# Kernel optimization log

Hardware: AMD Instinct MI355X
Metric: run time of the kernel (lower is better)

The kernel has to match this reference:

```python
import jax, jax.numpy as jnp
import numpy as np

B, LT, LI, D, H, K = 32, 512, 576, 768, 8, 512


def setup_inputs() -> dict:
    key = jax.random.key(0)
    ks = jax.random.split(key, 10)
    s = 0.02
    return {
        "text_hidden_states": jax.random.normal(ks[0], (B, LT, D), jnp.float32),
        "image_hidden_states": jax.random.normal(ks[1], (B, LI, D), jnp.float32),
        "text_mask": jnp.ones((B, LT), jnp.int32),
        "Wb": jax.random.normal(ks[2], (H, D, D), jnp.float32) * s,   # per-head Linear weights [out,in]
        "Wv": jax.random.normal(ks[3], (K, D), jnp.float32) * s,
        "Wq": jax.random.normal(ks[4], (K, D), jnp.float32) * s,
        "Whv": jax.random.normal(ks[5], (K,), jnp.float32) * s,
        "Whq": jax.random.normal(ks[6], (K,), jnp.float32) * s,
        "Wo": jax.random.normal(ks[7], (D, D * H), jnp.float32) * s,  # output_proj weight [out,in]
        "bo": jnp.zeros((D,), jnp.float32),
    }


def reference(text_hidden_states, image_hidden_states, text_mask, Wb, Wv, Wq, Whv, Whq, Wo, bo):
    text, image = text_hidden_states, image_hidden_states
    # per-head text projection (torch Linear: x @ W.T), batched over heads
    pt = jnp.einsum('bxe,hfe->hbxf', text, Wb)                 # [H,B,LT,D]
    aff = jnp.einsum('hbxe,bye->hbxy', pt, image)              # [H,B,LT,LI]
    wv_v = jnp.einsum('bye,ke->byk', image, Wv)                # [B,LI,K] (head-shared)
    wq_q = jnp.einsum('bxe,ke->bxk', text, Wq)                 # [B,LT,K]
    wqqc = jnp.einsum('bxk,hbxy->hbyk', wq_q, aff)             # [H,B,LI,K]
    wvvc = jnp.einsum('byk,hbxy->hbxk', wv_v, aff)             # [H,B,LT,K]
    h_v = jnp.tanh(wv_v[None] + wqqc)
    h_q = jnp.tanh(wq_q[None] + wvvc)
    att_v = jax.nn.softmax(jnp.einsum('hbyk,k->hby', h_v, Whv), axis=-1)  # over image tokens
    att_q = jax.nn.softmax(jnp.einsum('hbxk,k->hbx', h_q, Whq), axis=-1)  # over text tokens
    ctx_v = jnp.einsum('hby,byd->hbd', att_v, image)
    ctx_q = jnp.einsum('hbx,bxd->hbd', att_q, text)
    head_out = ctx_v + ctx_q                                   # [H,B,D]
    combined = jnp.transpose(head_out, (1, 0, 2)).reshape(text.shape[0], -1)  # [B,H*D]
    return combined @ Wo.T + bo
```

## Files before the change

kernel.cpp:

```cpp
#include <hip/hip_runtime.h>
#include <math.h>

#define B_  32
#define LT_ 512
#define LI_ 576
#define LIP 640
#define D_  768
#define H_  8
#define K_  512
#define NTOK  (LI_ + LT_)
#define CSPLIT 8
#define TPB   (NTOK / CSPLIT)
#define NHEAD ((long)H_ * B_ * D_)

typedef __attribute__((ext_vector_type(4))) short short4v;
typedef __attribute__((ext_vector_type(8))) unsigned short ushort8;
typedef __attribute__((ext_vector_type(8))) _Float16 f16x8;
typedef __attribute__((ext_vector_type(4))) float f32x4;

__device__ __forceinline__ unsigned short f2h(float x) {
  _Float16 h = (_Float16)x;
  return __builtin_bit_cast(unsigned short, h);
}
__device__ __forceinline__ float h2f(unsigned short u) {
  return (float)__builtin_bit_cast(_Float16, u);
}
__device__ __forceinline__ float ftanh(float x) {
  float e = __expf(2.f * x);
  return 1.f - 2.f * __builtin_amdgcn_rcpf(e + 1.f);
}

__device__ __forceinline__ void gl_lds16(const void* g, void* l) {
  __builtin_amdgcn_global_load_lds(
      (const __attribute__((address_space(1))) void*)g,
      (__attribute__((address_space(3))) void*)l, 16, 0, 0);
}

#define EPI_PLAIN 0
#define EPI_T     1
#define EPI_TANH  2
#define EPI_OUT   3

struct Seg {
  const unsigned short *A, *B;
  unsigned short *C, *CT;
  const unsigned short* base;
  const float* wvec;
  float* outv;
  long sA, sB, sC, sCT, sBase;
  int Kd, lda, ldb;
  int gx, gy, nblk, epi, Mlim, valid, ldc, ldt;
};
struct Params { Seg s0, s1, s2; };

__global__ __launch_bounds__(256, 2) void mfma_seg(Params p)
{
  const int orig = blockIdx.x, nwg = gridDim.x;
  const int q8 = nwg >> 3, r8 = nwg & 7;
  const int xcd = orig & 7, idx = orig >> 3;
  const int wg = (xcd < r8 ? xcd * (q8 + 1) : r8 * (q8 + 1) + (xcd - r8) * q8) + idx;

  Seg sg; int local;
  if (wg < p.s0.nblk)                      { sg = p.s0; local = wg; }
  else if (wg < p.s0.nblk + p.s1.nblk)     { sg = p.s1; local = wg - p.s0.nblk; }
  else                                     { sg = p.s2; local = wg - p.s0.nblk - p.s1.nblk; }

  const int bx = local % sg.gx;
  const int tmp2 = local / sg.gx;
  const int by = tmp2 % sg.gy, bz = tmp2 / sg.gy;

  __shared__ unsigned short LDSU[24576];

  const int t = threadIdx.x, lane = t & 63, w = t >> 6;
  const int wr = w >> 1, wc = w & 1;
  const int m0 = bx * 256, n0 = by * 128;
  const int Kd = sg.Kd, lda = sg.lda, ldb = sg.ldb, ldc = sg.ldc;
  const unsigned short* A  = sg.A + (long)bz * sg.sA;
  const unsigned short* Bm = sg.B + (long)bz * sg.sB;

  const int rowb = w * 16 + (lane >> 2);
  const int cswz = ((lane & 3) ^ ((rowb >> 1) & 3)) * 8;
  const bool clampA = (m0 + 256 > sg.Mlim);
  const unsigned short* aSrc = A  + (long)(m0 + rowb) * lda + cswz;
  const unsigned short* bSrc = Bm + (long)(n0 + rowb) * ldb + cswz;
  const int ldsLane = rowb * 32;

  f32x4 acc[8][4];
  #pragma unroll
  for (int i = 0; i < 8; ++i)
    #pragma unroll
    for (int j = 0; j < 4; ++j)
      acc[i][j] = (f32x4){0.f, 0.f, 0.f, 0.f};

  const int rl = lane & 15, g = lane >> 4;
  const int aslot = (g ^ ((rl >> 1) & 3)) << 3;

  auto stage = [&](int bufi, int k0) {
    unsigned short* Ab = LDSU + bufi * 12288;
    unsigned short* Bb = Ab + 8192;
    if (!clampA) {
      #pragma unroll
      for (int q = 0; q < 4; ++q)
        gl_lds16(aSrc + (long)q * 64 * lda + k0, Ab + ldsLane + q * 2048);
    } else {
      #pragma unroll
      for (int q = 0; q < 4; ++q) {
        int rgl = m0 + q * 64 + rowb;
        if (rgl >= sg.Mlim) rgl = sg.Mlim - 1;
        gl_lds16(A + (long)rgl * lda + cswz + k0, Ab + ldsLane + q * 2048);
      }
    }
    #pragma unroll
    for (int q = 0; q < 2; ++q)
      gl_lds16(bSrc + (long)q * 64 * ldb + k0, Bb + ldsLane + q * 2048);
  };

  const int nt = Kd >> 5;
  stage(0, 0);
  __syncthreads();
  int cur = 0;
  for (int tt = 0; tt < nt; ++tt) {
    if (tt + 1 < nt) stage(cur ^ 1, (tt + 1) << 5);
    const unsigned short* Ab = LDSU + cur * 12288;
    const unsigned short* Bb = Ab + 8192;
    f16x8 af[8], bf[4];
    #pragma unroll
    for (int i = 0; i < 8; ++i)
      af[i] = *(const f16x8*)&Ab[(wr * 128 + i * 16 + rl) * 32 + aslot];
    #pragma unroll
    for (int j = 0; j < 4; ++j)
      bf[j] = *(const f16x8*)&Bb[(wc * 64 + j * 16 + rl) * 32 + aslot];
    __builtin_amdgcn_s_setprio(1);
    #pragma unroll
    for (int i = 0; i < 8; ++i)
      #pragma unroll
      for (int j = 0; j < 4; ++j)
        acc[i][j] = __builtin_amdgcn_mfma_f32_16x16x32_f16(af[i], bf[j], acc[i][j], 0, 0, 0);
    __builtin_amdgcn_s_setprio(0);
    __syncthreads();
    cur ^= 1;
  }

  const int rg = lane >> 4;
  if (sg.epi <= EPI_T) {
    unsigned short* C = sg.C + (long)bz * sg.sC;
    #pragma unroll
    for (int i = 0; i < 8; ++i)
      #pragma unroll
      for (int j = 0; j < 4; ++j)
        #pragma unroll
        for (int rr = 0; rr < 4; ++rr) {
          int ml = wr * 128 + i * 16 + rg * 4 + rr;
          int nl = wc * 64 + j * 16 + rl;
          if (m0 + ml < sg.Mlim)
            C[(long)(m0 + ml) * ldc + n0 + nl] = f2h(acc[i][j][rr]);
        }
    if (sg.epi == EPI_T) {
      unsigned short* CT = sg.CT + (long)bz * sg.sCT;
      __syncthreads();
      #pragma unroll
      for (int pp = 0; pp < 2; ++pp) {
        if (wr == pp) {
          #pragma unroll
          for (int i = 0; i < 8; ++i)
            #pragma unroll
            for (int j = 0; j < 4; ++j) {
              int nl = wc * 64 + j * 16 + rl;
              int mh = i * 16 + rg * 4;
              *(short4v*)&LDSU[nl * 136 + mh] = (short4v){
                  (short)f2h(acc[i][j][0]), (short)f2h(acc[i][j][1]),
                  (short)f2h(acc[i][j][2]), (short)f2h(acc[i][j][3])};
            }
        }
        __syncthreads();
        #pragma unroll
        for (int rr = 0; rr < 8; ++rr) {
          int rn = rr * 16 + (t >> 4);
          int m8 = (t & 15) * 8;
          int mg = m0 + pp * 128 + m8;
          if (mg < sg.Mlim)
            *(ushort8*)(CT + (long)(n0 + rn) * sg.ldt + mg) =
                *(const ushort8*)&LDSU[rn * 136 + m8];
        }
        __syncthreads();
      }
    }
  } else if (sg.epi == EPI_TANH) {
    const unsigned short* base = sg.base + (long)bz * sg.sBase;
    float* outp = sg.outv + (long)bz * sg.valid;
    #pragma unroll
    for (int i = 0; i < 8; ++i)
      #pragma unroll
      for (int rr = 0; rr < 4; ++rr) {
        int row = m0 + wr * 128 + i * 16 + rg * 4 + rr;
        if (row < sg.Mlim) {
          float s = 0.f;
          #pragma unroll
          for (int j = 0; j < 4; ++j) {
            int col = n0 + wc * 64 + j * 16 + rl;
            float v = acc[i][j][rr] + h2f(base[(long)row * ldc + col]);
            s += ftanh(v) * sg.wvec[col];
          }
          s += __shfl_xor(s, 1, 64);
          s += __shfl_xor(s, 2, 64);
          s += __shfl_xor(s, 4, 64);
          s += __shfl_xor(s, 8, 64);
          if (rl == 0 && row < sg.valid)
            atomicAdd(&outp[row], s);
        }
      }
  } else {
    float* outp = sg.outv;
    if (wr == 0) {
      #pragma unroll
      for (int i = 0; i < 2; ++i)
        #pragma unroll
        for (int rr = 0; rr < 4; ++rr) {
          int row = i * 16 + rg * 4 + rr;
          #pragma unroll
          for (int j = 0; j < 4; ++j) {
            int col = n0 + wc * 64 + j * 16 + rl;
            atomicAdd(&outp[(long)row * ldc + col], acc[i][j][rr]);
          }
        }
    }
  }
}

struct CSeg { const float* src; unsigned short* dst; long n8; };

__global__ __launch_bounds__(256) void cast_multi(
    CSeg c0, CSeg c1, CSeg c2, CSeg c3, CSeg c4)
{
  long i = (long)blockIdx.x * 256 + threadIdx.x;
  const float* src; unsigned short* dst;
  if      (i < c0.n8)                 { src = c0.src; dst = c0.dst; }
  else if ((i -= c0.n8) < c1.n8)      { src = c1.src; dst = c1.dst; }
  else if ((i -= c1.n8) < c2.n8)      { src = c2.src; dst = c2.dst; }
  else if ((i -= c2.n8) < c3.n8)      { src = c3.src; dst = c3.dst; }
  else if ((i -= c3.n8) < c4.n8)      { src = c4.src; dst = c4.dst; }
  else return;
  float4 v0 = ((const float4*)src)[i * 2];
  float4 v1 = ((const float4*)src)[i * 2 + 1];
  ushort8 o;
  o[0] = f2h(v0.x); o[1] = f2h(v0.y); o[2] = f2h(v0.z); o[3] = f2h(v0.w);
  o[4] = f2h(v1.x); o[5] = f2h(v1.y); o[6] = f2h(v1.z); o[7] = f2h(v1.w);
  *(ushort8*)(dst + i * 8) = o;
}

__global__ __launch_bounds__(256) void cast_pad_image(
    const float* __restrict__ in, unsigned short* __restrict__ out)
{
  long tid = (long)blockIdx.x * 256 + threadIdx.x;
  const long tot = (long)B_ * LIP * (D_ / 8);
  if (tid >= tot) return;
  int e8 = (int)(tid % (D_ / 8));
  long rw = tid / (D_ / 8);
  int y  = (int)(rw % LIP);
  long b = rw / LIP;
  ushort8 o;
  if (y < LI_) {
    const float* p = in + ((b * LI_ + y) * D_ + e8 * 8);
    float4 v0 = *(const float4*)p, v1 = *(const float4*)(p + 4);
    o[0] = f2h(v0.x); o[1] = f2h(v0.y); o[2] = f2h(v0.z); o[3] = f2h(v0.w);
    o[4] = f2h(v1.x); o[5] = f2h(v1.y); o[6] = f2h(v1.z); o[7] = f2h(v1.w);
  } else {
    #pragma unroll
    for (int j = 0; j < 8; ++j) o[j] = 0;
  }
  *(ushort8*)(out + rw * D_ + e8 * 8) = o;
}

__global__ __launch_bounds__(256) void zero_f32(float* __restrict__ p, long n) {
  long i = (long)blockIdx.x * 256 + threadIdx.x;
  if (i < n) p[i] = 0.f;
}

__global__ __launch_bounds__(256) void init_out(
    const float* __restrict__ bo, float* __restrict__ out)
{
  int i = blockIdx.x * 256 + threadIdx.x;
  out[i] = bo[i % D_];
}

__global__ __launch_bounds__(256) void softmax_att(
    const float* __restrict__ lv, const float* __restrict__ lq,
    float* __restrict__ attvG, float* __restrict__ attqG)
{
  const int b = blockIdx.x, h = blockIdx.y;
  const int t = threadIdx.x;
  __shared__ float buf[LI_];
  __shared__ float red[4];

  const float* lvp = lv + ((long)h * B_ + b) * LI_;
  float m = -1e30f;
  for (int i = t; i < LI_; i += 256) m = fmaxf(m, lvp[i]);
  #pragma unroll
  for (int o = 32; o > 0; o >>= 1) m = fmaxf(m, __shfl_down(m, o, 64));
  if ((t & 63) == 0) red[t >> 6] = m;
  __syncthreads();
  m = fmaxf(fmaxf(red[0], red[1]), fmaxf(red[2], red[3]));
  __syncthreads();
  float s = 0.f;
  for (int i = t; i < LI_; i += 256) { float e = __expf(lvp[i] - m); buf[i] = e; s += e; }
  #pragma unroll
  for (int o = 32; o > 0; o >>= 1) s += __shfl_down(s, o, 64);
  if ((t & 63) == 0) red[t >> 6] = s;
  __syncthreads();
  s = red[0] + red[1] + red[2] + red[3];
  {
    float inv = 1.f / s;
    float* op = attvG + ((long)h * B_ + b) * LI_;
    for (int i = t; i < LI_; i += 256) op[i] = buf[i] * inv;
  }
  __syncthreads();

  const float* lqp = lq + ((long)h * B_ + b) * LT_;
  m = -1e30f;
  for (int i = t; i < LT_; i += 256) m = fmaxf(m, lqp[i]);
  #pragma unroll
  for (int o = 32; o > 0; o >>= 1) m = fmaxf(m, __shfl_down(m, o, 64));
  if ((t & 63) == 0) red[t >> 6] = m;
  __syncthreads();
  m = fmaxf(fmaxf(red[0], red[1]), fmaxf(red[2], red[3]));
  __syncthreads();
  s = 0.f;
  for (int i = t; i < LT_; i += 256) { float e = __expf(lqp[i] - m); buf[i] = e; s += e; }
  #pragma unroll
  for (int o = 32; o > 0; o >>= 1) s += __shfl_down(s, o, 64);
  if ((t & 63) == 0) red[t >> 6] = s;
  __syncthreads();
  s = red[0] + red[1] + red[2] + red[3];
  {
    float inv = 1.f / s;
    float* op = attqG + ((long)h * B_ + b) * LT_;
    for (int i = t; i < LT_; i += 256) op[i] = buf[i] * inv;
  }
}

__global__ __launch_bounds__(256) void ctx_part(
    const float* __restrict__ attvG, const float* __restrict__ attqG,
    const unsigned short* __restrict__ text_h,
    float* __restrict__ head_part)
{
  const int b = blockIdx.x, d0 = blockIdx.y * 128, s = blockIdx.z;
  const int t = threadIdx.x, dl = t & 127, g = t >> 7;
  const long IMG_OFF = (long)B_ * LT_ * D_;
  __shared__ float wts[H_][TPB];
  __shared__ long  roff[TPB];
  __shared__ float red[H_][128];
  const int tok0 = s * TPB;
  for (int i = t; i < H_ * TPB; i += 256) {
    int h = i / TPB, j = i % TPB, tok = tok0 + j;
    wts[h][j] = tok < LI_ ? attvG[((long)h * B_ + b) * LI_ + tok]
                          : attqG[((long)h * B_ + b) * LT_ + (tok - LI_)];
  }
  if (t < TPB) {
    int tok = tok0 + t;
    roff[t] = tok < LI_ ? IMG_OFF + ((long)b * LIP + tok) * D_
                        : ((long)b * LT_ + (tok - LI_)) * D_;
  }
  __syncthreads();
  float acc[H_];
  #pragma unroll
  for (int h = 0; h < H_; ++h) acc[h] = 0.f;
  #pragma unroll 4
  for (int j = g; j < TPB; j += 2) {
    float val = h2f(text_h[roff[j] + d0 + dl]);
    #pragma unroll
    for (int h = 0; h < H_; ++h) acc[h] = fmaf(wts[h][j], val, acc[h]);
  }
  if (g == 1) {
    #pragma unroll
    for (int h = 0; h < H_; ++h) red[h][dl] = acc[h];
  }
  __syncthreads();
  if (g == 0) {
    float* hp = head_part + (long)s * NHEAD;
    #pragma unroll
    for (int h = 0; h < H_; ++h)
      hp[((long)h * B_ + b) * D_ + d0 + dl] = acc[h] + red[h][dl];
  }
}

__global__ __launch_bounds__(256) void reduce_head(
    const float* __restrict__ head_part, unsigned short* __restrict__ head16)
{
  long i = (long)blockIdx.x * 256 + threadIdx.x;
  float s = 0.f;
  #pragma unroll
  for (int p = 0; p < CSPLIT; ++p) s += head_part[(long)p * NHEAD + i];
  int d = (int)(i % D_);
  long hb = i / D_;
  int b = (int)(hb % B_), h = (int)(hb / B_);
  head16[(long)b * (H_ * D_) + (long)h * D_ + d] = f2h(s);
}

extern "C" void kernel_launch(void* const* d_in, const int* in_sizes, int n_in,
                              void* d_out, int out_size, void* d_ws, size_t ws_size,
                              hipStream_t stream)
{
  const float* text  = (const float*)d_in[0];
  const float* image = (const float*)d_in[1];
  const float* Wb  = (const float*)d_in[3];
  const float* Wv  = (const float*)d_in[4];
  const float* Wq  = (const float*)d_in[5];
  const float* Whv = (const float*)d_in[6];
  const float* Whq = (const float*)d_in[7];
  const float* Wo  = (const float*)d_in[8];
  const float* bo  = (const float*)d_in[9];
  float* out = (float*)d_out;

  const long N_TEXT = (long)B_ * LT_ * D_;
  const long N_IMGP = (long)B_ * LIP * D_;
  const long N_WV   = (long)K_ * D_;
  const long N_WB   = (long)H_ * D_ * D_;
  const long N_WO   = (long)D_ * H_ * D_;
  const long N_WVV  = (long)B_ * LIP * K_;
  const long N_WQQ  = (long)B_ * LT_ * K_;
  const long N_PT   = (long)B_ * LT_ * D_;
  const long N_AFF  = (long)B_ * LT_ * LIP;
  const long N_LV   = (long)H_ * B_ * LI_;
  const long N_LQ   = (long)H_ * B_ * LT_;
  const long N_H16  = (long)B_ * H_ * D_;

  unsigned short* wsu = (unsigned short*)d_ws;
  long off = 0;
  unsigned short* text_h  = wsu + off; off += N_TEXT;
  unsigned short* image_p = wsu + off; off += N_IMGP;
  unsigned short* Wv_h    = wsu + off; off += N_WV;
  unsigned short* Wq_h    = wsu + off; off += N_WV;
  unsigned short* Wb_h    = wsu + off; off += N_WB;
  unsigned short* Wo_h    = wsu + off; off += N_WO;
  unsigned short* wv_v    = wsu + off; off += N_WVV;
  unsigned short* wq_q    = wsu + off; off += N_WQQ;
  unsigned short* wv_vT   = wsu + off; off += N_WVV;
  unsigned short* wq_qT   = wsu + off; off += N_WQQ;
  unsigned short* pt_h    = wsu + off; off += N_PT;
  unsigned short* aff     = wsu + off; off += N_AFF;
  unsigned short* affT    = wsu + off; off += N_AFF;
  unsigned short* head16  = wsu + off; off += N_H16;
  float* lv        = (float*)(wsu + off);
  float* lq        = lv + N_LV;
  float* attvG     = lq + N_LQ;
  float* attqG     = attvG + N_LV;
  float* head_part = attqG + N_LQ;
  const size_t need = (size_t)off * 2 +
      (size_t)(2 * (N_LV + N_LQ) + CSPLIT * NHEAD) * 4;
  if (ws_size < need) return;

  dim3 blk(256);

  {
    CSeg c0{text, text_h, N_TEXT / 8};
    CSeg c1{Wv,   Wv_h,   N_WV / 8};
    CSeg c2{Wq,   Wq_h,   N_WV / 8};
    CSeg c3{Wb,   Wb_h,   N_WB / 8};
    CSeg c4{Wo,   Wo_h,   N_WO / 8};
    long tot8 = c0.n8 + c1.n8 + c2.n8 + c3.n8 + c4.n8;
    cast_multi<<<(unsigned)((tot8 + 255) / 256), blk, 0, stream>>>(c0, c1, c2, c3, c4);
  }
  cast_pad_image<<<(unsigned)((B_ * LIP * (D_ / 8) + 255) / 256), blk, 0, stream>>>(image, image_p);
  zero_f32<<<(unsigned)((N_LV + N_LQ + 255) / 256), blk, 0, stream>>>(lv, N_LV + N_LQ);
  init_out<<<(unsigned)(B_ * D_ / 256), blk, 0, stream>>>(bo, out);

  Seg zs{};  zs.nblk = 0;

  {
    Seg s0{}; s0.A = image_p; s0.B = Wv_h; s0.C = wv_v; s0.CT = wv_vT;
    s0.sA = (long)LIP * D_; s0.sC = (long)LIP * K_; s0.sCT = (long)K_ * LIP;
    s0.Kd = D_; s0.lda = D_; s0.ldb = D_;
    s0.gx = 3; s0.gy = 4; s0.nblk = 3 * 4 * B_; s0.epi = EPI_T;
    s0.Mlim = LIP; s0.ldc = K_; s0.ldt = LIP;

    Seg s1{}; s1.A = text_h; s1.B = Wq_h; s1.C = wq_q; s1.CT = wq_qT;
    s1.sA = (long)LT_ * D_; s1.sC = (long)LT_ * K_; s1.sCT = (long)K_ * LT_;
    s1.Kd = D_; s1.lda = D_; s1.ldb = D_;
    s1.gx = 2; s1.gy = 4; s1.nblk = 2 * 4 * B_; s1.epi = EPI_T;
    s1.Mlim = LT_; s1.ldc = K_; s1.ldt = LT_;

    Seg s2{}; s2.A = text_h; s2.B = Wb_h; s2.C = pt_h;
    s2.Kd = D_; s2.lda = D_; s2.ldb = D_;
    s2.gx = 64; s2.gy = 6; s2.nblk = 64 * 6; s2.epi = EPI_PLAIN;
    s2.Mlim = B_ * LT_; s2.ldc = D_;

    Params P{s0, s1, s2};
    mfma_seg<<<s0.nblk + s1.nblk + s2.nblk, blk, 0, stream>>>(P);
  }

  for (int h = 0; h < H_; ++h) {
    {
      Seg s0{}; s0.A = pt_h; s0.B = image_p; s0.C = aff; s0.CT = affT;
      s0.sA = (long)LT_ * D_; s0.sB = (long)LIP * D_;
      s0.sC = (long)LT_ * LIP; s0.sCT = (long)LIP * LT_;
      s0.Kd = D_; s0.lda = D_; s0.ldb = D_;
      s0.gx = 2; s0.gy = 5; s0.nblk = 2 * 5 * B_; s0.epi = EPI_T;
      s0.Mlim = LT_; s0.ldc = LIP; s0.ldt = LT_;
      Params P{s0, zs, zs};
      mfma_seg<<<s0.nblk, blk, 0, stream>>>(P);
    }
    {
      Seg s0{}; s0.A = affT; s0.B = wq_qT;
      s0.base = wv_v; s0.wvec = Whv; s0.outv = lv + (long)h * B_ * LI_;
      s0.sA = (long)LIP * LT_; s0.sB = (long)K_ * LT_; s0.sBase = (long)LIP * K_;
      s0.Kd = LT_; s0.lda = LT_; s0.ldb = LT_;
      s0.gx = 3; s0.gy = 4; s0.nblk = 3 * 4 * B_; s0.epi = EPI_TANH;
      s0.Mlim = LIP; s0.valid = LI_; s0.ldc = K_;

      Seg s1{}; s1.A = aff; s1.B = wv_vT;
      s1.base = wq_q; s1.wvec = Whq; s1.outv = lq + (long)h * B_ * LT_;
      s1.sA = (long)LT_ * LIP; s1.sB = (long)K_ * LIP; s1.sBase = (long)LT_ * K_;
      s1.Kd = LIP; s1.lda = LIP; s1.ldb = LIP;
      s1.gx = 2; s1.gy = 4; s1.nblk = 2 * 4 * B_; s1.epi = EPI_TANH;
      s1.Mlim = LT_; s1.valid = LT_; s1.ldc = K_;

      Seg s2 = zs;
      if (h < H_ - 1) {
        s2.A = text_h; s2.B = Wb_h + (long)(h + 1) * D_ * D_; s2.C = pt_h;
        s2.Kd = D_; s2.lda = D_; s2.ldb = D_;
        s2.gx = 64; s2.gy = 6; s2.nblk = 64 * 6; s2.epi = EPI_PLAIN;
        s2.Mlim = B_ * LT_; s2.ldc = D_;
      }
      Params P{s0, s1, s2};
      mfma_seg<<<s0.nblk + s1.nblk + s2.nblk, blk, 0, stream>>>(P);
    }
  }

  softmax_att<<<dim3(B_, H_), blk, 0, stream>>>(lv, lq, attvG, attqG);
  ctx_part<<<dim3(B_, D_ / 128, CSPLIT), blk, 0, stream>>>(attvG, attqG, text_h, head_part);
  reduce_head<<<(unsigned)(NHEAD / 256), blk, 0, stream>>>(head_part, head16);

  {
    Seg s0{}; s0.A = head16; s0.B = Wo_h; s0.outv = out;
    s0.sA = (long)(H_ * D_ / 8); s0.sB = (long)(H_ * D_ / 8);
    s0.Kd = H_ * D_ / 8; s0.lda = H_ * D_; s0.ldb = H_ * D_;
    s0.gx = 1; s0.gy = 6; s0.nblk = 1 * 6 * 8; s0.epi = EPI_OUT;
    s0.Mlim = B_; s0.valid = B_; s0.ldc = D_;
    Params P{s0, zs, zs};
    mfma_seg<<<s0.nblk, blk, 0, stream>>>(P);
  }
}
```

Measured before the change: 1.060 ms.

## Triple-buffer GEMM LDS staging with explicit vmcnt waits and single barrier

Replaces the double-buffered K loop with a three-stage LDS ring: three tiles are prefetched up front and each iteration issues the load two tiles ahead. The end-of-iteration __syncthreads is replaced by a counted s_waitcnt vmcnt plus one s_barrier, and fragment reads now go through inline ds_read_b128 with an explicit lgkmcnt wait. The aim is to hide more global-load latency and cut barrier stalls between MFMA phases. The cost is 1.5x the LDS per block, which could limit occupancy, and a hand-counted wait scheme that breaks if the per-stage load count changes.

New measurement: 1.074 ms. No clear change (+1.4%).

```diff
diff --git a/kernel.cpp b/kernel.cpp
--- a/kernel.cpp
+++ b/kernel.cpp
@@ -36,6 +36,14 @@
       (__attribute__((address_space(3))) void*)l, 16, 0, 0);
 }
 
+__device__ __forceinline__ f16x8 lds_read16(const unsigned short* p) {
+  f16x8 r;
+  const __attribute__((address_space(3))) unsigned short* lp =
+      (const __attribute__((address_space(3))) unsigned short*)p;
+  asm volatile("ds_read_b128 %0, %1" : "=v"(r) : "v"(lp));
+  return r;
+}
+
 #define EPI_PLAIN 0
 #define EPI_T     1
 #define EPI_TANH  2
@@ -69,7 +77,7 @@
   const int tmp2 = local / sg.gx;
   const int by = tmp2 % sg.gy, bz = tmp2 / sg.gy;
 
-  __shared__ unsigned short LDSU[24576];
+  __shared__ unsigned short LDSU[36864];
 
   const int t = threadIdx.x, lane = t & 63, w = t >> 6;
   const int wr = w >> 1, wc = w & 1;
@@ -78,12 +86,12 @@
   const unsigned short* A  = sg.A + (long)bz * sg.sA;
   const unsigned short* Bm = sg.B + (long)bz * sg.sB;
 
-  const int rowb = w * 16 + (lane >> 2);
-  const int cswz = ((lane & 3) ^ ((rowb >> 1) & 3)) * 8;
+  const int srow = w * 16 + (lane >> 2);
+  const int cswz = ((lane & 3) ^ ((srow >> 1) & 3)) * 8;
   const bool clampA = (m0 + 256 > sg.Mlim);
-  const unsigned short* aSrc = A  + (long)(m0 + rowb) * lda + cswz;
-  const unsigned short* bSrc = Bm + (long)(n0 + rowb) * ldb + cswz;
-  const int ldsLane = rowb * 32;
+  const unsigned short* aSrc = A  + (long)(m0 + srow) * lda + cswz;
+  const unsigned short* bSrc = Bm + (long)(n0 + srow) * ldb + cswz;
+  const int ldsLane = w * 512 + lane * 8;
 
   f32x4 acc[8][4];
   #pragma unroll
@@ -105,7 +113,7 @@
     } else {
       #pragma unroll
       for (int q = 0; q < 4; ++q) {
-        int rgl = m0 + q * 64 + rowb;
+        int rgl = m0 + q * 64 + srow;
         if (rgl >= sg.Mlim) rgl = sg.Mlim - 1;
         gl_lds16(A + (long)rgl * lda + cswz + k0, Ab + ldsLane + q * 2048);
       }
@@ -115,21 +123,29 @@
       gl_lds16(bSrc + (long)q * 64 * ldb + k0, Bb + ldsLane + q * 2048);
   };
 
+  f16x8 af[8], bf[4];
+  auto ldfrags = [&](int bufi) {
+    const unsigned short* Ab = LDSU + bufi * 12288;
+    const unsigned short* Bb = Ab + 8192;
+    #pragma unroll
+    for (int i = 0; i < 8; ++i)
+      af[i] = lds_read16(&Ab[(wr * 128 + i * 16 + rl) * 32 + aslot]);
+    #pragma unroll
+    for (int j = 0; j < 4; ++j)
+      bf[j] = lds_read16(&Bb[(wc * 64 + j * 16 + rl) * 32 + aslot]);
+  };
+
   const int nt = Kd >> 5;
-  stage(0, 0);
-  __syncthreads();
-  int cur = 0;
+  stage(0, 0); stage(1, 32); stage(2, 64);
   for (int tt = 0; tt < nt; ++tt) {
-    if (tt + 1 < nt) stage(cur ^ 1, (tt + 1) << 5);
-    const unsigned short* Ab = LDSU + cur * 12288;
-    const unsigned short* Bb = Ab + 8192;
-    f16x8 af[8], bf[4];
-    #pragma unroll
-    for (int i = 0; i < 8; ++i)
-      af[i] = *(const f16x8*)&Ab[(wr * 128 + i * 16 + rl) * 32 + aslot];
-    #pragma unroll
-    for (int j = 0; j < 4; ++j)
-      bf[j] = *(const f16x8*)&Bb[(wc * 64 + j * 16 + rl) * 32 + aslot];
+    if (tt == 0)          asm volatile("s_waitcnt vmcnt(12)" ::: "memory");
+    else if (tt + 1 < nt) asm volatile("s_waitcnt vmcnt(6)"  ::: "memory");
+    else                  asm volatile("s_waitcnt vmcnt(0)"  ::: "memory");
+    __builtin_amdgcn_s_barrier();
+    ldfrags(tt % 3);
+    if (tt >= 1 && tt + 2 < nt) stage((tt - 1) % 3, (tt + 2) << 5);
+    asm volatile("s_waitcnt lgkmcnt(0)" ::: "memory");
+    __builtin_amdgcn_sched_barrier(0);
     __builtin_amdgcn_s_setprio(1);
     #pragma unroll
     for (int i = 0; i < 8; ++i)
@@ -137,8 +153,6 @@
       for (int j = 0; j < 4; ++j)
         acc[i][j] = __builtin_amdgcn_mfma_f32_16x16x32_f16(af[i], bf[j], acc[i][j], 0, 0, 0);
     __builtin_amdgcn_s_setprio(0);
-    __syncthreads();
-    cur ^= 1;
   }
 
   const int rg = lane >> 4;
```
